# Kernel tuning notes

Hardware: AMD Instinct MI355X
Metric: run time of the kernel (lower is better)

## Reference

```python
import jax, jax.numpy as jnp
import numpy as np

HIDDEN = 768
N_HEADS = 12
HEAD_DIM = HIDDEN // N_HEADS  # 64 (multihead=True)
NEG_BIG = -1e31


def setup_inputs() -> dict:
    key = jax.random.key(0)
    ks = jax.random.split(key, 8)
    B, S = 4, 2048
    toks = jax.random.normal(ks[0], (B, S, HIDDEN), dtype=jnp.float32)
    masks = jax.random.randint(ks[1], (B, S), 0, 2, dtype=jnp.int32)
    s = 0.02
    Wq = jax.random.normal(ks[2], (HIDDEN, HIDDEN), dtype=jnp.float32) * s
    Wk = jax.random.normal(ks[3], (HIDDEN, HIDDEN), dtype=jnp.float32) * s
    Wv = jax.random.normal(ks[4], (HIDDEN, HIDDEN), dtype=jnp.float32) * s
    bq = jax.random.normal(ks[5], (HIDDEN,), dtype=jnp.float32) * s
    bk = jax.random.normal(ks[6], (HIDDEN,), dtype=jnp.float32) * s
    bv = jax.random.normal(ks[7], (HIDDEN,), dtype=jnp.float32) * s
    return {"toks": toks, "masks": masks, "Wq": Wq, "bq": bq,
            "Wk": Wk, "bk": bk, "Wv": Wv, "bv": bv}


def reference(toks, masks, Wq, bq, Wk, bk, Wv, bv):
    B, S, D = toks.shape
    m = masks.astype(jnp.float32)  # [B,S]
    # additive outer-product padding mask: (1 - m_i*m_j) * -1e31, shape [B,S,S]
    add_mask = (1.0 - m[:, :, None] * m[:, None, :]) * NEG_BIG

    def split_heads(x):  # [B,S,D] -> [B,H,S,hd]
        return x.reshape(B, S, N_HEADS, HEAD_DIM).transpose(0, 2, 1, 3)

    q = split_heads(toks @ Wq + bq)
    k = split_heads(toks @ Wk + bk)
    v = split_heads(toks @ Wv + bv)

    scores = jnp.einsum("bhqd,bhkd->bhqk", q, k) / jnp.sqrt(
        jnp.asarray(HEAD_DIM, dtype=toks.dtype))
    scores = scores + add_mask[:, None, :, :]
    probs = jax.nn.softmax(scores, axis=-1)  # dropout is identity at eval
    ctx = jnp.einsum("bhqk,bhkd->bhqd", probs, v)
    return ctx.transpose(0, 2, 1, 3).reshape(B, S, D)
```

## Files before the change

kernel.cpp:

```cpp
#include <hip/hip_runtime.h>
#include <hip/hip_bf16.h>
#include <cstddef>


typedef __bf16 bf16_8 __attribute__((ext_vector_type(8)));
typedef float f32x4 __attribute__((ext_vector_type(4)));
typedef short s16x4 __attribute__((ext_vector_type(4)));
typedef short s16x8 __attribute__((ext_vector_type(8)));

#define HID 768
#define NHEADS 12
#define HD 64
#define BATCH 4
#define SEQ 2048
#define NEGBIG2 (-1.44269504e31f)
#define SCALE2 0.18033688f

#define KT 64
#define NKT (SEQ / KT)
#define STR 68
#define ASTR 72

static __device__ __forceinline__ f32x4 mfma16x16x32(bf16_8 a, bf16_8 b, f32x4 c) {
  return __builtin_amdgcn_mfma_f32_16x16x32_bf16(a, b, c, 0, 0, 0);
}

static __device__ __forceinline__ void lds_barrier() {
  __asm__ volatile("s_waitcnt lgkmcnt(0)\n\ts_barrier" ::: "memory");
}

static __device__ __forceinline__ float fast_exp2(float x) {
#if __has_builtin(__builtin_amdgcn_exp2f)
  return __builtin_amdgcn_exp2f(x);
#else
  return __expf(x * 0.69314718f);
#endif
}

static __device__ __forceinline__ s16x4 pack_bf16x4(f32x4 p) {
  s16x4 o;
#pragma unroll
  for (int i = 0; i < 4; ++i) {
    __bf16 b = (__bf16)p[i];
    o[i] = __builtin_bit_cast(short, b);
  }
  return o;
}

static __device__ __forceinline__ bf16_8 cat2(const __bf16* p) {
  s16x4 lo = *(const s16x4*)p;
  s16x4 hi = *(const s16x4*)(p + 4);
  s16x8 v = __builtin_shufflevector(lo, hi, 0, 1, 2, 3, 4, 5, 6, 7);
  return __builtin_bit_cast(bf16_8, v);
}

static __device__ __forceinline__ void write2(__bf16* p, s16x8 v) {
  *(s16x4*)p = __builtin_shufflevector(v, v, 0, 1, 2, 3);
  *(s16x4*)(p + 4) = __builtin_shufflevector(v, v, 4, 5, 6, 7);
}

static __device__ __forceinline__ bf16_8 cvt_a_frag(const float* p) {
  f32x4 af0 = *(const f32x4*)p;
  f32x4 af1 = *(const f32x4*)(p + 4);
  bf16_8 a;
  a[0] = (__bf16)af0[0]; a[1] = (__bf16)af0[1];
  a[2] = (__bf16)af0[2]; a[3] = (__bf16)af0[3];
  a[4] = (__bf16)af1[0]; a[5] = (__bf16)af1[1];
  a[6] = (__bf16)af1[2]; a[7] = (__bf16)af1[3];
  return a;
}

__global__ __launch_bounds__(256) void transpose768x3(const float* __restrict__ Wq,
                                                      const float* __restrict__ Wk,
                                                      const float* __restrict__ Wv,
                                                      __bf16* __restrict__ WtBase,
                                                      const int* __restrict__ masks,
                                                      float* __restrict__ kaddG) {
  int tx = threadIdx.x, ty = threadIdx.y;
  if (blockIdx.z == 3) {
    int fid = blockIdx.y * gridDim.x + blockIdx.x;
    if (fid < (BATCH * SEQ) / 256) {
      int i = fid * 256 + ty * 32 + tx;
      kaddG[i] = masks[i] ? 0.0f : NEGBIG2;
    }
    return;
  }
  const float* in = blockIdx.z == 0 ? Wq : (blockIdx.z == 1 ? Wk : Wv);
  __bf16* out = WtBase + (size_t)blockIdx.z * HID * HID;
  __shared__ __bf16 tile[32][33];
  int bx = blockIdx.x * 32, by = blockIdx.y * 32;
#pragma unroll
  for (int r = 0; r < 32; r += 8)
    tile[ty + r][tx] = (__bf16)in[(size_t)(by + ty + r) * HID + bx + tx];
  __syncthreads();
#pragma unroll
  for (int r = 0; r < 32; r += 8)
    out[(size_t)(bx + ty + r) * HID + by + tx] = tile[tx][ty + r];
}

__global__ __launch_bounds__(256, 5) void proj_kv(const float* __restrict__ toks,
                                                  const __bf16* __restrict__ WtK,
                                                  const float* __restrict__ bk,
                                                  const __bf16* __restrict__ WtV,
                                                  const float* __restrict__ bv,
                                                  __bf16* __restrict__ Kout,
                                                  __bf16* __restrict__ Vtout,
                                                  int head0, int hm) {
  __shared__ __align__(16) __bf16 ldsA[2][64 * ASTR];
  int tid = threadIdx.x;
  int w = tid >> 6, lane = tid & 63, l16 = lane & 15, quad = lane >> 4;
  int m0 = blockIdx.x * 64;
  int hl = blockIdx.y, h = head0 + hl;
  int srow = tid >> 2, scg = tid & 3;
  const float* asrc = toks + (size_t)(m0 + srow) * HID + scg * 8;
  const __bf16* bKrow = WtK + (size_t)(h * 64 + w * 16 + l16) * HID + quad * 8;
  const __bf16* bVrow = WtV + (size_t)(h * 64 + w * 16 + l16) * HID + quad * 8;
  f32x4 zero = {0.f, 0.f, 0.f, 0.f};
  f32x4 aK[4], aV[4];
#pragma unroll
  for (int mt = 0; mt < 4; ++mt) { aK[mt] = zero; aV[mt] = zero; }

  *(bf16_8*)(&ldsA[0][srow * ASTR + scg * 8]) = cvt_a_frag(asrc);
  *(bf16_8*)(&ldsA[0][srow * ASTR + 32 + scg * 8]) = cvt_a_frag(asrc + 32);
  __syncthreads();

  const int NCH = HID / 64;
  for (int t = 0; t < NCH; ++t) {
    int b = t & 1;
    int kk = t * 64;
    bf16_8 areg0, areg1;
    if (t + 1 < NCH) {
      areg0 = cvt_a_frag(asrc + kk + 64);
      areg1 = cvt_a_frag(asrc + kk + 96);
    }
    bf16_8 bkf0 = *(const bf16_8*)(bKrow + kk);
    bf16_8 bkf1 = *(const bf16_8*)(bKrow + kk + 32);
    bf16_8 bvf0 = *(const bf16_8*)(bVrow + kk);
    bf16_8 bvf1 = *(const bf16_8*)(bVrow + kk + 32);
    __builtin_amdgcn_s_setprio(1);
#pragma unroll
    for (int mt = 0; mt < 4; ++mt) {
      bf16_8 af0 = *(const bf16_8*)(&ldsA[b][(mt * 16 + l16) * ASTR + quad * 8]);
      bf16_8 af1 = *(const bf16_8*)(&ldsA[b][(mt * 16 + l16) * ASTR + 32 + quad * 8]);
      aK[mt] = mfma16x16x32(af0, bkf0, aK[mt]);
      aK[mt] = mfma16x16x32(af1, bkf1, aK[mt]);
      aV[mt] = mfma16x16x32(af0, bvf0, aV[mt]);
      aV[mt] = mfma16x16x32(af1, bvf1, aV[mt]);
    }
    __builtin_amdgcn_s_setprio(0);
    if (t + 1 < NCH) {
      *(bf16_8*)(&ldsA[b ^ 1][srow * ASTR + scg * 8]) = areg0;
      *(bf16_8*)(&ldsA[b ^ 1][srow * ASTR + 32 + scg * 8]) = areg1;
      lds_barrier();
    }
  }

  int d = w * 16 + l16;
  float bnK = bk[h * 64 + d];
  float bnV = bv[h * 64 + d];
#pragma unroll
  for (int mt = 0; mt < 4; ++mt) {
#pragma unroll
    for (int r = 0; r < 4; ++r) {
      int m = m0 + mt * 16 + quad * 4 + r;
      int b = m >> 11;
      int s = m & (SEQ - 1);
      Kout[(((size_t)b * hm + hl) * SEQ + s) * HD + d] = (__bf16)(aK[mt][r] + bnK);
      Vtout[(((size_t)b * hm + hl) * HD + d) * SEQ + s] = (__bf16)(aV[mt][r] + bnV);
    }
  }
}

__global__ __launch_bounds__(256, 3) void attn_fused(const float* __restrict__ toks,
                                                     const __bf16* __restrict__ WtQ,
                                                     const float* __restrict__ bq,
                                                     const __bf16* __restrict__ Kbuf,
                                                     const __bf16* __restrict__ Vtbuf,
                                                     const float* __restrict__ kaddG,
                                                     float* __restrict__ out,
                                                     int head0, int hm) {
  __shared__ __align__(16) __bf16 ldsK[2][64 * STR];
  __shared__ __align__(16) __bf16 ldsV[2][64 * STR];
  __shared__ __align__(16) __bf16 ldsQP[64 * STR];
  int tid = threadIdx.x;
  int w = tid >> 6, lane = tid & 63, l16 = lane & 15, quad = lane >> 4;

  int nwg = gridDim.x * gridDim.y * gridDim.z;
  int hwf = blockIdx.x + gridDim.x * (blockIdx.y + gridDim.y * blockIdx.z);
  int lg = (hwf & 7) * (nwg >> 3) + (hwf >> 3);
  int q0 = (lg & (gridDim.x - 1)) * 64;
  int grp = lg / gridDim.x;
  int hl = grp % hm, bz = grp / hm;
  int h = head0 + hl;

  const float* kb = kaddG + (size_t)bz * SEQ;
  f32x4 zero = {0.f, 0.f, 0.f, 0.f};

  const __bf16* Kb = Kbuf + ((size_t)bz * hm + hl) * SEQ * HD;
  const __bf16* Vb = Vtbuf + ((size_t)bz * hm + hl) * HD * SEQ;

  {
    const float* arow = toks + ((size_t)bz * SEQ + q0 + w * 16 + l16) * HID + quad * 8;
    const __bf16* brow = WtQ + (size_t)(h * 64 + l16) * HID + quad * 8;
    f32x4 qa[4] = {zero, zero, zero, zero};
    for (int kk = 0; kk < HID; kk += 32) {
      bf16_8 a = cvt_a_frag(arow + kk);
#pragma unroll
      for (int t = 0; t < 4; ++t)
        qa[t] = mfma16x16x32(a, *(const bf16_8*)(brow + (size_t)t * 16 * HID + kk), qa[t]);
    }
#pragma unroll
    for (int t = 0; t < 4; ++t) {
      float bn = bq[h * 64 + t * 16 + l16];
#pragma unroll
      for (int r = 0; r < 4; ++r)
        ldsQP[(w * 16 + quad * 4 + r) * STR + t * 16 + l16] = (__bf16)(qa[t][r] + bn);
    }
  }

  int srow = tid >> 3, sc = tid & 7;
  {
    s16x8 k0 = *(const s16x8*)(Kb + (size_t)srow * HD + sc * 8);
    s16x8 k1 = *(const s16x8*)(Kb + (size_t)(srow + 32) * HD + sc * 8);
    s16x8 v0 = *(const s16x8*)(Vb + (size_t)srow * SEQ + sc * 8);
    s16x8 v1 = *(const s16x8*)(Vb + (size_t)(srow + 32) * SEQ + sc * 8);
    write2(&ldsK[0][srow * STR + sc * 8], k0);
    write2(&ldsK[0][(srow + 32) * STR + sc * 8], k1);
    write2(&ldsV[0][srow * STR + sc * 8], v0);
    write2(&ldsV[0][(srow + 32) * STR + sc * 8], v1);
  }
  __syncthreads();

  bf16_8 qf[4][2];
#pragma unroll
  for (int s = 0; s < 4; ++s)
#pragma unroll
    for (int half = 0; half < 2; ++half)
      qf[s][half] = cat2(&ldsQP[(s * 16 + l16) * STR + half * 32 + quad * 8]);
  float actq[4];
#pragma unroll
  for (int s = 0; s < 4; ++s) actq[s] = (kb[q0 + s * 16 + l16] == 0.0f) ? 1.0f : 0.0f;
  __syncthreads();

  float lsum[4] = {0.f, 0.f, 0.f, 0.f};
  f32x4 acc[4];
#pragma unroll
  for (int s = 0; s < 4; ++s) acc[s] = zero;

  for (int t = 0; t < NKT; ++t) {
    int j0 = t * KT;
    int jn = (t + 1 < NKT) ? j0 + KT : 0;
    int buf = t & 1, nbuf = buf ^ 1;
    s16x8 k0 = *(const s16x8*)(Kb + (size_t)(jn + srow) * HD + sc * 8);
    s16x8 k1 = *(const s16x8*)(Kb + (size_t)(jn + srow + 32) * HD + sc * 8);
    s16x8 v0 = *(const s16x8*)(Vb + (size_t)srow * SEQ + jn + sc * 8);
    s16x8 v1 = *(const s16x8*)(Vb + (size_t)(srow + 32) * SEQ + jn + sc * 8);

    bf16_8 kf0 = cat2(&ldsK[buf][(w * 16 + l16) * STR + quad * 8]);
    bf16_8 kf1 = cat2(&ldsK[buf][(w * 16 + l16) * STR + 32 + quad * 8]);
    f32x4 ck = *(const f32x4*)(kb + j0 + w * 16 + quad * 4);
    __builtin_amdgcn_s_setprio(1);
#pragma unroll
    for (int s = 0; s < 4; ++s) {
      f32x4 st = mfma16x16x32(kf1, qf[s][1], mfma16x16x32(kf0, qf[s][0], zero));
      f32x4 p;
#pragma unroll
      for (int r = 0; r < 4; ++r) {
        float v = actq[s] * fmaf(st[r], SCALE2, ck[r]);
        p[r] = fast_exp2(v);
      }
      lsum[s] += p[0] + p[1] + p[2] + p[3];
      *(s16x4*)(&ldsQP[(s * 16 + l16) * STR + w * 16 + quad * 4]) = pack_bf16x4(p);
    }
    __builtin_amdgcn_s_setprio(0);
    lds_barrier();

    __builtin_amdgcn_s_setprio(1);
#pragma unroll
    for (int kc = 0; kc < 2; ++kc) {
      bf16_8 vf = cat2(&ldsV[buf][(w * 16 + l16) * STR + kc * 32 + quad * 8]);
#pragma unroll
      for (int s = 0; s < 4; ++s) {
        bf16_8 pf = cat2(&ldsQP[(s * 16 + l16) * STR + kc * 32 + quad * 8]);
        acc[s] = mfma16x16x32(pf, vf, acc[s]);
      }
    }
    __builtin_amdgcn_s_setprio(0);
    write2(&ldsK[nbuf][srow * STR + sc * 8], k0);
    write2(&ldsK[nbuf][(srow + 32) * STR + sc * 8], k1);
    write2(&ldsV[nbuf][srow * STR + sc * 8], v0);
    write2(&ldsV[nbuf][(srow + 32) * STR + sc * 8], v1);
    lds_barrier();
  }

  __syncthreads();
  float* ls = (float*)ldsQP;
#pragma unroll
  for (int s = 0; s < 4; ++s) {
    float v = lsum[s];
    v += __shfl_xor(v, 16);
    v += __shfl_xor(v, 32);
    if (quad == 0) ls[(w * 4 + s) * 16 + l16] = v;
  }
  __syncthreads();
  float lr[4][4];
#pragma unroll
  for (int s = 0; s < 4; ++s) {
    float tot = ls[(0 * 4 + s) * 16 + l16] + ls[(1 * 4 + s) * 16 + l16] +
                ls[(2 * 4 + s) * 16 + l16] + ls[(3 * 4 + s) * 16 + l16];
    float linv = 1.0f / tot;
#pragma unroll
    for (int r = 0; r < 4; ++r) lr[s][r] = __shfl(linv, quad * 4 + r);
  }
#pragma unroll
  for (int s = 0; s < 4; ++s)
#pragma unroll
    for (int r = 0; r < 4; ++r)
      out[((size_t)bz * SEQ + q0 + s * 16 + quad * 4 + r) * HID + h * HD + w * 16 + l16] =
          acc[s][r] * lr[s][r];
}

extern "C" void kernel_launch(void* const* d_in, const int* in_sizes, int n_in,
                              void* d_out, int out_size, void* d_ws, size_t ws_size,
                              hipStream_t stream) {
  (void)in_sizes; (void)n_in; (void)out_size;
  const float* toks = (const float*)d_in[0];
  const int* masks = (const int*)d_in[1];
  const float* Wq = (const float*)d_in[2];
  const float* bq = (const float*)d_in[3];
  const float* Wk = (const float*)d_in[4];
  const float* bk = (const float*)d_in[5];
  const float* Wv = (const float*)d_in[6];
  const float* bv = (const float*)d_in[7];
  char* ws = (char*)d_ws;
  const size_t KADD_B = (size_t)BATCH * SEQ * 4;
  const size_t WT_B = (size_t)HID * HID * 2;
  const size_t KV_FULL_B = (size_t)BATCH * NHEADS * SEQ * HD * 2;
  const size_t KV_HEAD_B = (size_t)BATCH * SEQ * HD * 2;
  const size_t TIER_A_NEED = KADD_B + 3 * WT_B + 2 * KV_FULL_B;
  float* kaddG = (float*)(ws);
  __bf16* WtQ = (__bf16*)(ws + KADD_B + 0 * WT_B);
  __bf16* WtK = (__bf16*)(ws + KADD_B + 1 * WT_B);
  __bf16* WtV = (__bf16*)(ws + KADD_B + 2 * WT_B);
  float* outp = (float*)d_out;

  dim3 tgrid(HID / 32, HID / 32, 4), tblk(32, 8);
  transpose768x3<<<tgrid, tblk, 0, stream>>>(Wq, Wk, Wv, WtQ, masks, kaddG);

  if (ws_size >= TIER_A_NEED) {
    __bf16* Kf = (__bf16*)(ws + KADD_B + 3 * WT_B);
    __bf16* Vtf = (__bf16*)(ws + KADD_B + 3 * WT_B + KV_FULL_B);
    dim3 pgrid(BATCH * SEQ / 64, NHEADS);
    proj_kv<<<pgrid, 256, 0, stream>>>(toks, WtK, bk, WtV, bv, Kf, Vtf, 0, NHEADS);
    dim3 agrid(SEQ / 64, NHEADS, BATCH);
    attn_fused<<<agrid, 256, 0, stream>>>(toks, WtQ, bq, Kf, Vtf, kaddG, outp, 0, NHEADS);
  } else {
    __bf16* Kh = (__bf16*)(ws + KADD_B + 3 * WT_B);
    __bf16* Vth = (__bf16*)(ws + KADD_B + 3 * WT_B + KV_HEAD_B);
    dim3 pgrid(BATCH * SEQ / 64, 1);
    dim3 agrid(SEQ / 64, 1, BATCH);
    for (int h = 0; h < NHEADS; ++h) {
      proj_kv<<<pgrid, 256, 0, stream>>>(toks, WtK, bk, WtV, bv, Kh, Vth, h, 1);
      attn_fused<<<agrid, 256, 0, stream>>>(toks, WtQ, bq, Kh, Vth, kaddG, outp, h, 1);
    }
  }
}
```

Measured before the change: 308.2 us.

## Rewrite attention as single-wave 32x32 MFMA kernel with async LDS loads and bitmask

The attention kernel now runs one 64-thread wave per 64-query tile instead of four waves. It uses 32x32x16 MFMAs, keeps P in registers via permlane32 swaps instead of staging it through LDS, and streams K/V into swizzled LDS double buffers with global_load_lds, which removes the block barriers. The padding mask becomes a packed bitmask read with readlane, replacing the per-key float additive array. The cost is less parallelism per workgroup, more register pressure, and reliance on hand-written waitcnt ordering.

New measurement: 433.5 us. 40.6% more time.

```diff
diff --git a/kernel.cpp b/kernel.cpp
--- a/kernel.cpp
+++ b/kernel.cpp
@@ -5,8 +5,10 @@
 
 typedef __bf16 bf16_8 __attribute__((ext_vector_type(8)));
 typedef float f32x4 __attribute__((ext_vector_type(4)));
+typedef float f32x16 __attribute__((ext_vector_type(16)));
 typedef short s16x4 __attribute__((ext_vector_type(4)));
 typedef short s16x8 __attribute__((ext_vector_type(8)));
+typedef unsigned int u32x4 __attribute__((ext_vector_type(4)));
 
 #define HID 768
 #define NHEADS 12
@@ -16,17 +18,33 @@
 #define NEGBIG2 (-1.44269504e31f)
 #define SCALE2 0.18033688f
 
-#define KT 64
-#define NKT (SEQ / KT)
-#define STR 68
+#define KVB 64
+#define NKT (SEQ / KVB)
+#define STRQ 68
 #define ASTR 72
 
 static __device__ __forceinline__ f32x4 mfma16x16x32(bf16_8 a, bf16_8 b, f32x4 c) {
   return __builtin_amdgcn_mfma_f32_16x16x32_bf16(a, b, c, 0, 0, 0);
 }
+static __device__ __forceinline__ f32x16 mfma32x32x16(bf16_8 a, bf16_8 b, f32x16 c) {
+  return __builtin_amdgcn_mfma_f32_32x32x16_bf16(a, b, c, 0, 0, 0);
+}
+
+static __device__ __forceinline__ void pl32swap(unsigned& a, unsigned& b) {
+  asm("v_permlane32_swap_b32 %0, %1" : "+v"(a), "+v"(b));
+}
+
+static __device__ __forceinline__ void gll16(const __bf16* g, __bf16* l) {
+  __builtin_amdgcn_global_load_lds(
+      (const __attribute__((address_space(1))) void*)g,
+      (__attribute__((address_space(3))) void*)l, 16, 0, 0);
+}
 
 static __device__ __forceinline__ void lds_barrier() {
   __asm__ volatile("s_waitcnt lgkmcnt(0)\n\ts_barrier" ::: "memory");
+}
+static __device__ __forceinline__ void lds_flush() {
+  __asm__ volatile("s_waitcnt lgkmcnt(0)" ::: "memory");
 }
 
 static __device__ __forceinline__ float fast_exp2(float x) {
@@ -37,14 +55,10 @@
 #endif
 }
 
-static __device__ __forceinline__ s16x4 pack_bf16x4(f32x4 p) {
-  s16x4 o;
-#pragma unroll
-  for (int i = 0; i < 4; ++i) {
-    __bf16 b = (__bf16)p[i];
-    o[i] = __builtin_bit_cast(short, b);
-  }
-  return o;
+static __device__ __forceinline__ unsigned pkbf(float a, float b) {
+  unsigned lo = (unsigned)__builtin_bit_cast(unsigned short, (__bf16)a);
+  unsigned hi = (unsigned)__builtin_bit_cast(unsigned short, (__bf16)b);
+  return lo | (hi << 16);
 }
 
 static __device__ __forceinline__ bf16_8 cat2(const __bf16* p) {
@@ -52,11 +66,6 @@
   s16x4 hi = *(const s16x4*)(p + 4);
   s16x8 v = __builtin_shufflevector(lo, hi, 0, 1, 2, 3, 4, 5, 6, 7);
   return __builtin_bit_cast(bf16_8, v);
-}
-
-static __device__ __forceinline__ void write2(__bf16* p, s16x8 v) {
-  *(s16x4*)p = __builtin_shufflevector(v, v, 0, 1, 2, 3);
-  *(s16x4*)(p + 4) = __builtin_shufflevector(v, v, 4, 5, 6, 7);
 }
 
 static __device__ __forceinline__ bf16_8 cvt_a_frag(const float* p) {
@@ -75,13 +84,17 @@
                                                       const float* __restrict__ Wv,
                                                       __bf16* __restrict__ WtBase,
                                                       const int* __restrict__ masks,
-                                                      float* __restrict__ kaddG) {
+                                                      unsigned* __restrict__ mbits) {
   int tx = threadIdx.x, ty = threadIdx.y;
   if (blockIdx.z == 3) {
     int fid = blockIdx.y * gridDim.x + blockIdx.x;
-    if (fid < (BATCH * SEQ) / 256) {
-      int i = fid * 256 + ty * 32 + tx;
-      kaddG[i] = masks[i] ? 0.0f : NEGBIG2;
+    if (fid == 0) {
+      int w = ty * 32 + tx;
+      const int* mp = masks + w * 32;
+      unsigned v = 0;
+#pragma unroll
+      for (int j = 0; j < 32; ++j) v |= (mp[j] ? 1u : 0u) << j;
+      mbits[w] = v;
     }
     return;
   }
@@ -137,7 +150,6 @@
     bf16_8 bkf1 = *(const bf16_8*)(bKrow + kk + 32);
     bf16_8 bvf0 = *(const bf16_8*)(bVrow + kk);
     bf16_8 bvf1 = *(const bf16_8*)(bVrow + kk + 32);
-    __builtin_amdgcn_s_setprio(1);
 #pragma unroll
     for (int mt = 0; mt < 4; ++mt) {
       bf16_8 af0 = *(const bf16_8*)(&ldsA[b][(mt * 16 + l16) * ASTR + quad * 8]);
@@ -147,7 +159,6 @@
       aV[mt] = mfma16x16x32(af0, bvf0, aV[mt]);
       aV[mt] = mfma16x16x32(af1, bvf1, aV[mt]);
     }
-    __builtin_amdgcn_s_setprio(0);
     if (t + 1 < NCH) {
       *(bf16_8*)(&ldsA[b ^ 1][srow * ASTR + scg * 8]) = areg0;
       *(bf16_8*)(&ldsA[b ^ 1][srow * ASTR + 32 + scg * 8]) = areg1;
@@ -171,19 +182,17 @@
   }
 }
 
-__global__ __launch_bounds__(256, 3) void attn_fused(const float* __restrict__ toks,
-                                                     const __bf16* __restrict__ WtQ,
-                                                     const float* __restrict__ bq,
-                                                     const __bf16* __restrict__ Kbuf,
-                                                     const __bf16* __restrict__ Vtbuf,
-                                                     const float* __restrict__ kaddG,
-                                                     float* __restrict__ out,
-                                                     int head0, int hm) {
-  __shared__ __align__(16) __bf16 ldsK[2][64 * STR];
-  __shared__ __align__(16) __bf16 ldsV[2][64 * STR];
-  __shared__ __align__(16) __bf16 ldsQP[64 * STR];
-  int tid = threadIdx.x;
-  int w = tid >> 6, lane = tid & 63, l16 = lane & 15, quad = lane >> 4;
+__global__ __launch_bounds__(64) void attn_fused(const float* __restrict__ toks,
+                                                 const __bf16* __restrict__ WtQ,
+                                                 const float* __restrict__ bq,
+                                                 const __bf16* __restrict__ Kbuf,
+                                                 const __bf16* __restrict__ Vtbuf,
+                                                 const unsigned* __restrict__ mbits,
+                                                 float* __restrict__ out,
+                                                 int head0, int hm) {
+  __shared__ __align__(16) __bf16 L[16384];
+  int lane = threadIdx.x & 63;
+  int l16 = lane & 15, quad = lane >> 4, l32 = lane & 31, hi = lane >> 5;
 
   int nwg = gridDim.x * gridDim.y * gridDim.z;
   int hwf = blockIdx.x + gridDim.x * (blockIdx.y + gridDim.y * blockIdx.z);
@@ -193,14 +202,14 @@
   int hl = grp % hm, bz = grp / hm;
   int h = head0 + hl;
 
-  const float* kb = kaddG + (size_t)bz * SEQ;
   f32x4 zero = {0.f, 0.f, 0.f, 0.f};
-
   const __bf16* Kb = Kbuf + ((size_t)bz * hm + hl) * SEQ * HD;
   const __bf16* Vb = Vtbuf + ((size_t)bz * hm + hl) * HD * SEQ;
 
-  {
-    const float* arow = toks + ((size_t)bz * SEQ + q0 + w * 16 + l16) * HID + quad * 8;
+  __bf16* Qs = L;
+#pragma unroll
+  for (int qs = 0; qs < 4; ++qs) {
+    const float* arow = toks + ((size_t)bz * SEQ + q0 + qs * 16 + l16) * HID + quad * 8;
     const __bf16* brow = WtQ + (size_t)(h * 64 + l16) * HID + quad * 8;
     f32x4 qa[4] = {zero, zero, zero, zero};
     for (int kk = 0; kk < HID; kk += 32) {
@@ -214,110 +223,145 @@
       float bn = bq[h * 64 + t * 16 + l16];
 #pragma unroll
       for (int r = 0; r < 4; ++r)
-        ldsQP[(w * 16 + quad * 4 + r) * STR + t * 16 + l16] = (__bf16)(qa[t][r] + bn);
-    }
-  }
-
-  int srow = tid >> 3, sc = tid & 7;
-  {
-    s16x8 k0 = *(const s16x8*)(Kb + (size_t)srow * HD + sc * 8);
-    s16x8 k1 = *(const s16x8*)(Kb + (size_t)(srow + 32) * HD + sc * 8);
-    s16x8 v0 = *(const s16x8*)(Vb + (size_t)srow * SEQ + sc * 8);
-    s16x8 v1 = *(const s16x8*)(Vb + (size_t)(srow + 32) * SEQ + sc * 8);
-    write2(&ldsK[0][srow * STR + sc * 8], k0);
-    write2(&ldsK[0][(srow + 32) * STR + sc * 8], k1);
-    write2(&ldsV[0][srow * STR + sc * 8], v0);
-    write2(&ldsV[0][(srow + 32) * STR + sc * 8], v1);
-  }
-  __syncthreads();
-
-  bf16_8 qf[4][2];
-#pragma unroll
-  for (int s = 0; s < 4; ++s)
-#pragma unroll
-    for (int half = 0; half < 2; ++half)
-      qf[s][half] = cat2(&ldsQP[(s * 16 + l16) * STR + half * 32 + quad * 8]);
-  float actq[4];
-#pragma unroll
-  for (int s = 0; s < 4; ++s) actq[s] = (kb[q0 + s * 16 + l16] == 0.0f) ? 1.0f : 0.0f;
-  __syncthreads();
-
-  float lsum[4] = {0.f, 0.f, 0.f, 0.f};
-  f32x4 acc[4];
-#pragma unroll
-  for (int s = 0; s < 4; ++s) acc[s] = zero;
+        Qs[(qs * 16 + quad * 4 + r) * STRQ + t * 16 + l16] = (__bf16)(qa[t][r] + bn);
+    }
+  }
+  lds_flush();
+
+  bf16_8 qf[2][4];
+#pragma unroll
+  for (int qsub = 0; qsub < 2; ++qsub)
+#pragma unroll
+    for (int c = 0; c < 4; ++c)
+      qf[qsub][c] = cat2(&Qs[(qsub * 32 + l32) * STRQ + c * 16 + hi * 8]);
+  lds_flush();
+
+  unsigned mask_all = mbits[bz * 64 + lane];
+  unsigned qw0 = (unsigned)__builtin_amdgcn_readlane((int)mask_all, (q0 >> 5));
+  unsigned qw1 = (unsigned)__builtin_amdgcn_readlane((int)mask_all, (q0 >> 5) + 1);
+  bool act0 = (qw0 >> l32) & 1u;
+  bool act1 = (qw1 >> l32) & 1u;
+  float sm0 = act0 ? SCALE2 : 0.0f;
+  float sm1 = act1 ? SCALE2 : 0.0f;
+  __asm__ volatile("" ::: "memory");
+
+  int drow = lane >> 3, dch = lane & 7;
+  int dswz = (dch ^ drow) * 8;
+  const __bf16* kSrc = Kb + (size_t)drow * HD + dswz;
+  const __bf16* vSrc = Vb + (size_t)drow * SEQ + dswz;
+  int xkh = (l32 >> 1) & 3;
+  int e0 = (hi ^ (l32 & 1)) << 3;
+  int o0 = ((0 ^ xkh) << 4) + e0;
+  int o1 = ((1 ^ xkh) << 4) + e0;
+  int o2 = ((2 ^ xkh) << 4) + e0;
+  int o3 = ((3 ^ xkh) << 4) + e0;
+
+#pragma unroll
+  for (int i = 0; i < 8; ++i) gll16(kSrc + (size_t)(i * 8) * HD, &L[0 + i * 512]);
+#pragma unroll
+  for (int i = 0; i < 8; ++i) gll16(vSrc + (size_t)(i * 8) * SEQ + 0, &L[8192 + i * 512]);
+#pragma unroll
+  for (int i = 0; i < 8; ++i) gll16(kSrc + (size_t)(KVB + i * 8) * HD, &L[4096 + i * 512]);
+#pragma unroll
+  for (int i = 0; i < 8; ++i) gll16(vSrc + (size_t)(i * 8) * SEQ + KVB, &L[12288 + i * 512]);
+
+  float lsum0 = 0.f, lsum1 = 0.f;
+  f32x16 acc00, acc01, acc10, acc11;
+#pragma unroll
+  for (int i = 0; i < 16; ++i) { acc00[i] = 0.f; acc01[i] = 0.f; acc10[i] = 0.f; acc11[i] = 0.f; }
 
   for (int t = 0; t < NKT; ++t) {
-    int j0 = t * KT;
-    int jn = (t + 1 < NKT) ? j0 + KT : 0;
-    int buf = t & 1, nbuf = buf ^ 1;
-    s16x8 k0 = *(const s16x8*)(Kb + (size_t)(jn + srow) * HD + sc * 8);
-    s16x8 k1 = *(const s16x8*)(Kb + (size_t)(jn + srow + 32) * HD + sc * 8);
-    s16x8 v0 = *(const s16x8*)(Vb + (size_t)srow * SEQ + jn + sc * 8);
-    s16x8 v1 = *(const s16x8*)(Vb + (size_t)(srow + 32) * SEQ + jn + sc * 8);
-
-    bf16_8 kf0 = cat2(&ldsK[buf][(w * 16 + l16) * STR + quad * 8]);
-    bf16_8 kf1 = cat2(&ldsK[buf][(w * 16 + l16) * STR + 32 + quad * 8]);
-    f32x4 ck = *(const f32x4*)(kb + j0 + w * 16 + quad * 4);
-    __builtin_amdgcn_s_setprio(1);
-#pragma unroll
-    for (int s = 0; s < 4; ++s) {
-      f32x4 st = mfma16x16x32(kf1, qf[s][1], mfma16x16x32(kf0, qf[s][0], zero));
-      f32x4 p;
-#pragma unroll
-      for (int r = 0; r < 4; ++r) {
-        float v = actq[s] * fmaf(st[r], SCALE2, ck[r]);
-        p[r] = fast_exp2(v);
+    int bufB = (t & 1) << 12;
+    __asm__ volatile("s_waitcnt vmcnt(16)" ::: "memory");
+    const __bf16* LK = L + bufB;
+    const __bf16* LV = L + 8192 + bufB;
+    unsigned m0w = (unsigned)__builtin_amdgcn_readlane((int)mask_all, 2 * t);
+    unsigned m1w = (unsigned)__builtin_amdgcn_readlane((int)mask_all, 2 * t + 1);
+    unsigned mh0 = m0w >> (hi * 4);
+    unsigned mh1 = m1w >> (hi * 4);
+#pragma unroll
+    for (int s = 0; s < 2; ++s) {
+      unsigned mhs = s ? mh1 : mh0;
+      int krow = (s * 32 + l32) * 64;
+      bf16_8 kf0 = *(const bf16_8*)(LK + krow + o0);
+      bf16_8 kf1 = *(const bf16_8*)(LK + krow + o1);
+      bf16_8 kf2 = *(const bf16_8*)(LK + krow + o2);
+      bf16_8 kf3 = *(const bf16_8*)(LK + krow + o3);
+      bf16_8 vf00 = *(const bf16_8*)(LV + (l32)*64 + (s ? o2 : o0));
+      bf16_8 vf01 = *(const bf16_8*)(LV + (l32)*64 + (s ? o3 : o1));
+      bf16_8 vf10 = *(const bf16_8*)(LV + (32 + l32) * 64 + (s ? o2 : o0));
+      bf16_8 vf11 = *(const bf16_8*)(LV + (32 + l32) * 64 + (s ? o3 : o1));
+#pragma unroll
+      for (int qsub = 0; qsub < 2; ++qsub) {
+        f32x16 st;
+#pragma unroll
+        for (int i = 0; i < 16; ++i) st[i] = 0.f;
+        st = mfma32x32x16(kf0, qf[qsub][0], st);
+        st = mfma32x32x16(kf1, qf[qsub][1], st);
+        st = mfma32x32x16(kf2, qf[qsub][2], st);
+        st = mfma32x32x16(kf3, qf[qsub][3], st);
+        bool aq = qsub ? act1 : act0;
+        float smq = qsub ? sm1 : sm0;
+        unsigned gate = aq ? ~mhs : 0u;
+        unsigned wds[8];
+        float ls = 0.f;
+#pragma unroll
+        for (int g = 0; g < 4; ++g) {
+          float ck0 = (gate & (1u << (8 * g + 0))) ? NEGBIG2 : 0.0f;
+          float ck1 = (gate & (1u << (8 * g + 1))) ? NEGBIG2 : 0.0f;
+          float ck2 = (gate & (1u << (8 * g + 2))) ? NEGBIG2 : 0.0f;
+          float ck3 = (gate & (1u << (8 * g + 3))) ? NEGBIG2 : 0.0f;
+          float p0 = fast_exp2(fmaf(st[g * 4 + 0], smq, ck0));
+          float p1 = fast_exp2(fmaf(st[g * 4 + 1], smq, ck1));
+          float p2 = fast_exp2(fmaf(st[g * 4 + 2], smq, ck2));
+          float p3 = fast_exp2(fmaf(st[g * 4 + 3], smq, ck3));
+          ls += (p0 + p1) + (p2 + p3);
+          wds[g * 2] = pkbf(p0, p1);
+          wds[g * 2 + 1] = pkbf(p2, p3);
+        }
+        if (qsub) lsum1 += ls; else lsum0 += ls;
+        pl32swap(wds[0], wds[2]);
+        pl32swap(wds[1], wds[3]);
+        pl32swap(wds[4], wds[6]);
+        pl32swap(wds[5], wds[7]);
+        u32x4 pd0 = {wds[0], wds[1], wds[2], wds[3]};
+        u32x4 pd1 = {wds[4], wds[5], wds[6], wds[7]};
+        bf16_8 pa0 = __builtin_bit_cast(bf16_8, pd0);
+        bf16_8 pa1 = __builtin_bit_cast(bf16_8, pd1);
+        if (qsub == 0) {
+          acc00 = mfma32x32x16(pa1, vf01, mfma32x32x16(pa0, vf00, acc00));
+          acc01 = mfma32x32x16(pa1, vf11, mfma32x32x16(pa0, vf10, acc01));
+        } else {
+          acc10 = mfma32x32x16(pa1, vf01, mfma32x32x16(pa0, vf00, acc10));
+          acc11 = mfma32x32x16(pa1, vf11, mfma32x32x16(pa0, vf10, acc11));
+        }
       }
-      lsum[s] += p[0] + p[1] + p[2] + p[3];
-      *(s16x4*)(&ldsQP[(s * 16 + l16) * STR + w * 16 + quad * 4]) = pack_bf16x4(p);
-    }
-    __builtin_amdgcn_s_setprio(0);
-    lds_barrier();
-
-    __builtin_amdgcn_s_setprio(1);
-#pragma unroll
-    for (int kc = 0; kc < 2; ++kc) {
-      bf16_8 vf = cat2(&ldsV[buf][(w * 16 + l16) * STR + kc * 32 + quad * 8]);
-#pragma unroll
-      for (int s = 0; s < 4; ++s) {
-        bf16_8 pf = cat2(&ldsQP[(s * 16 + l16) * STR + kc * 32 + quad * 8]);
-        acc[s] = mfma16x16x32(pf, vf, acc[s]);
-      }
-    }
-    __builtin_amdgcn_s_setprio(0);
-    write2(&ldsK[nbuf][srow * STR + sc * 8], k0);
-    write2(&ldsK[nbuf][(srow + 32) * STR + sc * 8], k1);
-    write2(&ldsV[nbuf][srow * STR + sc * 8], v0);
-    write2(&ldsV[nbuf][(srow + 32) * STR + sc * 8], v1);
-    lds_barrier();
-  }
-
-  __syncthreads();
-  float* ls = (float*)ldsQP;
-#pragma unroll
-  for (int s = 0; s < 4; ++s) {
-    float v = lsum[s];
-    v += __shfl_xor(v, 16);
+    }
+    __asm__ volatile("s_waitcnt lgkmcnt(0)" ::: "memory");
+    int jd = ((t + 2) & (NKT - 1)) * KVB;
+#pragma unroll
+    for (int i = 0; i < 8; ++i)
+      gll16(kSrc + (size_t)(jd + i * 8) * HD, &L[bufB + i * 512]);
+#pragma unroll
+    for (int i = 0; i < 8; ++i)
+      gll16(vSrc + (size_t)(i * 8) * SEQ + jd, &L[8192 + bufB + i * 512]);
+  }
+  __asm__ volatile("s_waitcnt vmcnt(0)" ::: "memory");
+
+#pragma unroll
+  for (int qsub = 0; qsub < 2; ++qsub) {
+    float v = qsub ? lsum1 : lsum0;
     v += __shfl_xor(v, 32);
-    if (quad == 0) ls[(w * 4 + s) * 16 + l16] = v;
-  }
-  __syncthreads();
-  float lr[4][4];
-#pragma unroll
-  for (int s = 0; s < 4; ++s) {
-    float tot = ls[(0 * 4 + s) * 16 + l16] + ls[(1 * 4 + s) * 16 + l16] +
-                ls[(2 * 4 + s) * 16 + l16] + ls[(3 * 4 + s) * 16 + l16];
-    float linv = 1.0f / tot;
-#pragma unroll
-    for (int r = 0; r < 4; ++r) lr[s][r] = __shfl(linv, quad * 4 + r);
-  }
-#pragma unroll
-  for (int s = 0; s < 4; ++s)
-#pragma unroll
-    for (int r = 0; r < 4; ++r)
-      out[((size_t)bz * SEQ + q0 + s * 16 + quad * 4 + r) * HID + h * HD + w * 16 + l16] =
-          acc[s][r] * lr[s][r];
+    float linv = 1.0f / v;
+#pragma unroll
+    for (int r = 0; r < 16; ++r) {
+      int row = (r & 3) + 8 * (r >> 2) + 4 * hi;
+      float sc = __shfl(linv, row);
+      size_t orow = (size_t)bz * SEQ + q0 + qsub * 32 + row;
+      out[orow * HID + h * HD + l32] = (qsub ? acc10[r] : acc00[r]) * sc;
+      out[orow * HID + h * HD + 32 + l32] = (qsub ? acc11[r] : acc01[r]) * sc;
+    }
+  }
 }
 
 extern "C" void kernel_launch(void* const* d_in, const int* in_sizes, int n_in,
@@ -333,35 +377,35 @@
   const float* Wv = (const float*)d_in[6];
   const float* bv = (const float*)d_in[7];
   char* ws = (char*)d_ws;
-  const size_t KADD_B = (size_t)BATCH * SEQ * 4;
+  const size_t MB_B = 1024;
   const size_t WT_B = (size_t)HID * HID * 2;
   const size_t KV_FULL_B = (size_t)BATCH * NHEADS * SEQ * HD * 2;
   const size_t KV_HEAD_B = (size_t)BATCH * SEQ * HD * 2;
-  const size_t TIER_A_NEED = KADD_B + 3 * WT_B + 2 * KV_FULL_B;
-  float* kaddG = (float*)(ws);
-  __bf16* WtQ = (__bf16*)(ws + KADD_B + 0 * WT_B);
-  __bf16* WtK = (__bf16*)(ws + KADD_B + 1 * WT_B);
-  __bf16* WtV = (__bf16*)(ws + KADD_B + 2 * WT_B);
+  const size_t TIER_A_NEED = MB_B + 3 * WT_B + 2 * KV_FULL_B;
+  unsigned* mbits = (unsigned*)(ws);
+  __bf16* WtQ = (__bf16*)(ws + MB_B + 0 * WT_B);
+  __bf16* WtK = (__bf16*)(ws + MB_B + 1 * WT_B);
+  __bf16* WtV = (__bf16*)(ws + MB_B + 2 * WT_B);
   float* outp = (float*)d_out;
 
   dim3 tgrid(HID / 32, HID / 32, 4), tblk(32, 8);
-  transpose768x3<<<tgrid, tblk, 0, stream>>>(Wq, Wk, Wv, WtQ, masks, kaddG);
+  transpose768x3<<<tgrid, tblk, 0, stream>>>(Wq, Wk, Wv, WtQ, masks, mbits);
 
   if (ws_size >= TIER_A_NEED) {
-    __bf16* Kf = (__bf16*)(ws + KADD_B + 3 * WT_B);
-    __bf16* Vtf = (__bf16*)(ws + KADD_B + 3 * WT_B + KV_FULL_B);
+    __bf16* Kf = (__bf16*)(ws + MB_B + 3 * WT_B);
+    __bf16* Vtf = (__bf16*)(ws + MB_B + 3 * WT_B + KV_FULL_B);
     dim3 pgrid(BATCH * SEQ / 64, NHEADS);
     proj_kv<<<pgrid, 256, 0, stream>>>(toks, WtK, bk, WtV, bv, Kf, Vtf, 0, NHEADS);
     dim3 agrid(SEQ / 64, NHEADS, BATCH);
-    attn_fused<<<agrid, 256, 0, stream>>>(toks, WtQ, bq, Kf, Vtf, kaddG, outp, 0, NHEADS);
+    attn_fused<<<agrid, 64, 0, stream>>>(toks, WtQ, bq, Kf, Vtf, mbits, outp, 0, NHEADS);
   } else {
-    __bf16* Kh = (__bf16*)(ws + KADD_B + 3 * WT_B);
-    __bf16* Vth = (__bf16*)(ws + KADD_B + 3 * WT_B + KV_HEAD_B);
+    __bf16* Kh = (__bf16*)(ws + MB_B + 3 * WT_B);
+    __bf16* Vth = (__bf16*)(ws + MB_B + 3 * WT_B + KV_HEAD_B);
     dim3 pgrid(BATCH * SEQ / 64, 1);
     dim3 agrid(SEQ / 64, 1, BATCH);
     for (int h = 0; h < NHEADS; ++h) {
       proj_kv<<<pgrid, 256, 0, stream>>>(toks, WtK, bk, WtV, bv, Kh, Vth, h, 1);
-      attn_fused<<<agrid, 256, 0, stream>>>(toks, WtQ, bq, Kh, Vth, kaddG, outp, h, 1);
-    }
-  }
-}
+      attn_fused<<<agrid, 64, 0, stream>>>(toks, WtQ, bq, Kh, Vth, mbits, outp, h, 1);
+    }
+  }
+}
```
